# Performance work log

Measured on AMD Instinct MI355X. Metric: run time of the kernel, lower is better.

Reference implementation:

```python
import jax, jax.numpy as jnp
import numpy as np


def _filters(bmt):
    # bmt: (L,) low-pass h(-m1..m2). dec_lo = flip(h); g_tilde = flip(h)*(-1)^j;
    # dec_hi = flip(g_tilde)  (matches bmt_h / bmt_g_tilde / bmt_g in the torch code)
    L = bmt.shape[0]
    signs = 1.0 - 2.0 * (jnp.arange(L) % 2).astype(bmt.dtype)  # (+1,-1,+1,...)
    dec_lo = jnp.flip(bmt)
    g_tilde = dec_lo * signs
    dec_hi = jnp.flip(g_tilde)
    return dec_lo, dec_hi


def _conv_stride2(xp, w):
    # xp: (B,1,Npad), w: (L,) -> cross-correlation, stride 2, valid (== torch conv1d)
    return jax.lax.conv_general_dilated(xp, w[None, None, :], window_strides=(2,), padding='VALID')


def _dwt(x, dec_lo, dec_hi, m1, m2):
    # x: (B,K,N) -> (a, d) each (B,K,N//2). Periodic padding:
    # pad_periodic(x,n1,n2)[i] = x[(i-n1) mod N]  ==  jnp.pad mode='wrap'.
    B, K, N = x.shape
    xr = x.reshape(B * K, 1, N)
    xa = jnp.pad(xr, ((0, 0), (0, 0), (m1, m2)), mode='wrap')
    a = _conv_stride2(xa, dec_lo)
    xd = jnp.pad(xr, ((0, 0), (0, 0), (m2 - 1, m1 + 1)), mode='wrap')
    d = _conv_stride2(xd, dec_hi)
    return a.reshape(B, K, N // 2), d.reshape(B, K, N // 2)


def setup_inputs() -> dict:
    key = jax.random.key(0)
    k1, k2 = jax.random.split(key)
    x = jax.random.normal(k1, (32, 1024, 1024), dtype=jnp.float32)
    bmt = jax.random.normal(k2, (8,), dtype=jnp.float32)
    return {"x": x, "bmt": bmt, "m1": 3, "m2": 4}


def reference(x, bmt, m1, m2):
    # 2D fast wavelet transform in square format (Wav_2d_sqformat)
    dec_lo, dec_hi = _filters(bmt)
    cA, cD = _dwt(x, dec_lo, dec_hi, m1, m2)                       # rows filtered
    cAA, cAD = _dwt(cA.swapaxes(1, 2), dec_lo, dec_hi, m1, m2)     # cols of cA
    cDA, cDD = _dwt(cD.swapaxes(1, 2), dec_lo, dec_hi, m1, m2)     # cols of cD
    cAA, cAD = cAA.swapaxes(1, 2), cAD.swapaxes(1, 2)
    cDA, cDD = cDA.swapaxes(1, 2), cDD.swapaxes(1, 2)
    top = jnp.concatenate([cAA, cAD], axis=2)
    bot = jnp.concatenate([cDA, cDD], axis=2)
    return jnp.concatenate([top, bot], axis=1)  # (B,N,N)
```

## Files before the change

### kernel.cpp

```cpp
#include <hip/hip_runtime.h>

#define NN 1024
#define HH 512
#define TR 32
#define TC 32
#define S1R 72
#define LST 33

__global__ __launch_bounds__(256, 8) void dwt2d_fused(const float* __restrict__ x,
                                                      const float* __restrict__ bmt,
                                                      float* __restrict__ out) {
    __shared__ float A1s[S1R][LST];
    __shared__ float D1s[S1R][LST];

    const int tid = threadIdx.x;
    const int b  = blockIdx.z;
    const int R0 = blockIdx.y * TR;
    const int C0 = blockIdx.x * TC;

    float lo[8], hi[8];
#pragma unroll
    for (int j = 0; j < 8; ++j) lo[j] = bmt[7 - j];
#pragma unroll
    for (int j = 0; j < 8; ++j) { float v = bmt[j]; hi[j] = (j & 1) ? v : -v; }

    const float* xb = x + (size_t)b * NN * NN;
    const int rbase = 2 * R0 - 3;
    const int gcol0 = 2 * C0 - 4;
    const bool interior = (gcol0 >= 0) && (gcol0 + 72 <= NN);

    for (int idx = tid; idx < S1R * 8; idx += 256) {
        int u  = idx >> 3;
        int cg = idx & 7;
        int row = (rbase + u) & (NN - 1);
        const float* xr = xb + (size_t)row * NN;
        int gb = gcol0 + 8 * cg;
        float p[16];
        if (interior) {
            const float4* xv = (const float4*)(xr + gb);
#pragma unroll
            for (int q = 0; q < 4; ++q) {
                float4 v = xv[q];
                p[4*q+0] = v.x; p[4*q+1] = v.y; p[4*q+2] = v.z; p[4*q+3] = v.w;
            }
        } else {
#pragma unroll
            for (int t = 0; t < 16; ++t) p[t] = xr[(gb + t) & (NN - 1)];
        }
#pragma unroll
        for (int i = 0; i < 4; ++i) {
            float a = 0.f, d = 0.f;
#pragma unroll
            for (int j = 0; j < 8; ++j) {
                float v = p[2*i + 1 + j];
                a += lo[j] * v;
                d += hi[j] * v;
            }
            A1s[u][4*cg + i] = a;
            D1s[u][4*cg + i] = d;
        }
    }
    __syncthreads();

    const int c  = tid & 31;
    const int r0 = tid >> 5;
    float* ob = out + (size_t)b * NN * NN;
#pragma unroll
    for (int k = 0; k < TR / 8; ++k) {
        int r = r0 + k * 8;
        float aa = 0.f, ad = 0.f, da = 0.f, dd = 0.f;
#pragma unroll
        for (int j = 0; j < 8; ++j) {
            float a1 = A1s[2 * r + j][c];
            float d1 = D1s[2 * r + j][c];
            aa += lo[j] * a1;
            ad += hi[j] * a1;
            da += lo[j] * d1;
            dd += hi[j] * d1;
        }
        int orow = R0 + r;
        int ocol = C0 + c;
        ob[(size_t)orow * NN + ocol]             = aa;
        ob[(size_t)orow * NN + ocol + HH]        = ad;
        ob[(size_t)(orow + HH) * NN + ocol]      = da;
        ob[(size_t)(orow + HH) * NN + ocol + HH] = dd;
    }
}

extern "C" void kernel_launch(void* const* d_in, const int* in_sizes, int n_in,
                              void* d_out, int out_size, void* d_ws, size_t ws_size,
                              hipStream_t stream) {
    const float* x   = (const float*)d_in[0];
    const float* bmt = (const float*)d_in[1];
    float* out = (float*)d_out;
    const int B = in_sizes[0] / (NN * NN);
    dim3 grid(HH / TC, HH / TR, B);
    dwt2d_fused<<<grid, 256, 0, stream>>>(x, bmt, out);
}
```

Baseline: 273.5 us.

## Stage input tile in LDS with coalesced float4 loads and vectorize output stores

```diff
diff --git a/kernel.cpp b/kernel.cpp
--- a/kernel.cpp
+++ b/kernel.cpp
@@ -4,14 +4,17 @@
 #define HH 512
 #define TR 32
 #define TC 32
-#define S1R 72
-#define LST 33
+#define S1R 70
+#define XC 72
+#define XST 73
+#define NF4 18
+#define NLD ((S1R * NF4 + 255) / 256)
 
-__global__ __launch_bounds__(256, 8) void dwt2d_fused(const float* __restrict__ x,
+__global__ __launch_bounds__(256, 4) void dwt2d_fused(const float* __restrict__ x,
                                                       const float* __restrict__ bmt,
                                                       float* __restrict__ out) {
-    __shared__ float A1s[S1R][LST];
-    __shared__ float D1s[S1R][LST];
+    __shared__ float  Xs[S1R][XST];
+    __shared__ float2 AD[S1R][TC + 2];
 
     const int tid = threadIdx.x;
     const int b  = blockIdx.z;
@@ -26,65 +29,77 @@
 
     const float* xb = x + (size_t)b * NN * NN;
     const int rbase = 2 * R0 - 3;
-    const int gcol0 = 2 * C0 - 4;
-    const bool interior = (gcol0 >= 0) && (gcol0 + 72 <= NN);
+    const int pb    = 2 * C0 - 4;
 
-    for (int idx = tid; idx < S1R * 8; idx += 256) {
-        int u  = idx >> 3;
-        int cg = idx & 7;
-        int row = (rbase + u) & (NN - 1);
-        const float* xr = xb + (size_t)row * NN;
-        int gb = gcol0 + 8 * cg;
-        float p[16];
-        if (interior) {
-            const float4* xv = (const float4*)(xr + gb);
+    float4 v[NLD];
+    int    su[NLD], stc[NLD];
 #pragma unroll
-            for (int q = 0; q < 4; ++q) {
-                float4 v = xv[q];
-                p[4*q+0] = v.x; p[4*q+1] = v.y; p[4*q+2] = v.z; p[4*q+3] = v.w;
-            }
-        } else {
+    for (int k = 0; k < NLD; ++k) {
+        int idx = tid + 256 * k;
+        unsigned uu = (unsigned)idx / 18u;
+        int tt = idx - 18 * (int)uu;
+        su[k] = (int)uu; stc[k] = tt;
+        int row = (rbase + (int)uu) & (NN - 1);
+        int gc  = (pb + 4 * tt) & (NN - 1);
+        v[k] = *(const float4*)(xb + ((size_t)row << 10) + gc);
+    }
 #pragma unroll
-            for (int t = 0; t < 16; ++t) p[t] = xr[(gb + t) & (NN - 1)];
-        }
-#pragma unroll
-        for (int i = 0; i < 4; ++i) {
-            float a = 0.f, d = 0.f;
-#pragma unroll
-            for (int j = 0; j < 8; ++j) {
-                float v = p[2*i + 1 + j];
-                a += lo[j] * v;
-                d += hi[j] * v;
-            }
-            A1s[u][4*cg + i] = a;
-            D1s[u][4*cg + i] = d;
+    for (int k = 0; k < NLD; ++k) {
+        int idx = tid + 256 * k;
+        if (idx < S1R * NF4) {
+            int u = su[k], t4 = 4 * stc[k];
+            Xs[u][t4 + 0] = v[k].x;
+            Xs[u][t4 + 1] = v[k].y;
+            Xs[u][t4 + 2] = v[k].z;
+            Xs[u][t4 + 3] = v[k].w;
         }
     }
     __syncthreads();
 
-    const int c  = tid & 31;
-    const int r0 = tid >> 5;
+    for (int pos = tid; pos < S1R * 8; pos += 256) {
+        int u  = pos >> 3;
+        int c0 = (pos & 7) * 4;
+        float p[14];
+#pragma unroll
+        for (int t = 0; t < 14; ++t) p[t] = Xs[u][2 * c0 + 1 + t];
+#pragma unroll
+        for (int m = 0; m < 4; ++m) {
+            float a = 0.f, d = 0.f;
+#pragma unroll
+            for (int j = 0; j < 8; ++j) {
+                float w = p[2 * m + j];
+                a += lo[j] * w;
+                d += hi[j] * w;
+            }
+            AD[u][c0 + m] = make_float2(a, d);
+        }
+    }
+    __syncthreads();
+
+    const int cg = tid & 7;
+    const int r  = tid >> 3;
+    float aa[4] = {0,0,0,0}, ad[4] = {0,0,0,0}, da[4] = {0,0,0,0}, dd[4] = {0,0,0,0};
+#pragma unroll
+    for (int j = 0; j < 8; ++j) {
+        float2 q[4];
+#pragma unroll
+        for (int i = 0; i < 4; ++i) q[i] = AD[2 * r + j][4 * cg + i];
+        float l = lo[j], h = hi[j];
+#pragma unroll
+        for (int i = 0; i < 4; ++i) {
+            aa[i] += l * q[i].x;
+            ad[i] += h * q[i].x;
+            da[i] += l * q[i].y;
+            dd[i] += h * q[i].y;
+        }
+    }
     float* ob = out + (size_t)b * NN * NN;
-#pragma unroll
-    for (int k = 0; k < TR / 8; ++k) {
-        int r = r0 + k * 8;
-        float aa = 0.f, ad = 0.f, da = 0.f, dd = 0.f;
-#pragma unroll
-        for (int j = 0; j < 8; ++j) {
-            float a1 = A1s[2 * r + j][c];
-            float d1 = D1s[2 * r + j][c];
-            aa += lo[j] * a1;
-            ad += hi[j] * a1;
-            da += lo[j] * d1;
-            dd += hi[j] * d1;
-        }
-        int orow = R0 + r;
-        int ocol = C0 + c;
-        ob[(size_t)orow * NN + ocol]             = aa;
-        ob[(size_t)orow * NN + ocol + HH]        = ad;
-        ob[(size_t)(orow + HH) * NN + ocol]      = da;
-        ob[(size_t)(orow + HH) * NN + ocol + HH] = dd;
-    }
+    const int orow = R0 + r;
+    const int ocol = C0 + 4 * cg;
+    *(float4*)(ob + (size_t)orow * NN + ocol)             = make_float4(aa[0], aa[1], aa[2], aa[3]);
+    *(float4*)(ob + (size_t)orow * NN + ocol + HH)        = make_float4(ad[0], ad[1], ad[2], ad[3]);
+    *(float4*)(ob + (size_t)(orow + HH) * NN + ocol)      = make_float4(da[0], da[1], da[2], da[3]);
+    *(float4*)(ob + (size_t)(orow + HH) * NN + ocol + HH) = make_float4(dd[0], dd[1], dd[2], dd[3]);
 }
 
 extern "C" void kernel_launch(void* const* d_in, const int* in_sizes, int n_in,
```

Result: faster. 234.2 us (-14.4%).
